# Kernel tuning notes

Measured on AMD Instinct MI355X. Metric: run time of the kernel, lower is better.

The kernel has to match this reference:

```python
import jax, jax.numpy as jnp
import numpy as np

ATT_UNITS = 64
DEC_DIM = 512
ENC_DIM = 512


def setup_inputs() -> dict:
    key = jax.random.key(0)
    k1, k2, k3, k4, k5 = jax.random.split(key, 5)
    B, S = 256, 512
    # glorot-uniform-ish init scales
    def glorot(k, shape):
        fan_in, fan_out = shape[0], shape[1]
        lim = np.sqrt(6.0 / (fan_in + fan_out))
        return jax.random.uniform(k, shape, jnp.float32, -lim, lim)
    return {
        "decoder_hidden_state": jax.random.normal(k1, (B, DEC_DIM), jnp.float32),
        "encoder_output": jax.random.normal(k2, (B, S, ENC_DIM), jnp.float32),
        "w1_kernel": glorot(k3, (DEC_DIM, ATT_UNITS)),
        "w1_bias": jnp.zeros((ATT_UNITS,), jnp.float32),
        "w2_kernel": glorot(k4, (ENC_DIM, ATT_UNITS)),
        "w2_bias": jnp.zeros((ATT_UNITS,), jnp.float32),
        "v_kernel": glorot(k5, (ATT_UNITS, 1)),
        "v_bias": jnp.zeros((1,), jnp.float32),
    }


def reference(decoder_hidden_state, encoder_output, w1_kernel, w1_bias,
              w2_kernel, w2_bias, v_kernel, v_bias):
    # dec proj: [B, 1, U]; enc proj: [B, S, U]
    dec = (decoder_hidden_state @ w1_kernel + w1_bias)[:, None, :]
    enc = jnp.einsum('bse,eu->bsu', encoder_output, w2_kernel) + w2_bias
    # score: [B, S, 1]
    score = jnp.tanh(dec + enc) @ v_kernel + v_bias
    att_weights = jax.nn.softmax(score, axis=1)  # softmax over sequence axis
    # weighted sum over S -> [B, E]
    context_vector = jnp.sum(att_weights * encoder_output, axis=1)
    return (context_vector, att_weights)
```

## Files before the change

kernel.cpp:

```cpp
#include <hip/hip_runtime.h>
#include <hip/hip_bf16.h>

constexpr int NB = 256;
constexpr int SQ = 512;
constexpr int ED = 512;
constexpr int DD = 512;
constexpr int UU = 64;
constexpr int NT = 32;

typedef __attribute__((ext_vector_type(8))) short bf16x8;
typedef __attribute__((ext_vector_type(4))) float f32x4;

__device__ __forceinline__ void stage16(const void* g, void* l) {
  __builtin_amdgcn_global_load_lds(
      (const __attribute__((address_space(1))) void*)g,
      (__attribute__((address_space(3))) void*)l, 16, 0, 0);
}

__device__ __forceinline__ unsigned short bf16_rne(float f) {
  unsigned int u = __float_as_uint(f);
  u += 0x7FFFu + ((u >> 16) & 1u);
  return (unsigned short)(u >> 16);
}

__device__ __forceinline__ unsigned int pack2(float lo, float hi) {
  __hip_bfloat162 h = __float22bfloat162_rn(make_float2(lo, hi));
  return *reinterpret_cast<unsigned int*>(&h);
}

constexpr size_t WS_DEC   = 131072;
constexpr size_t WS_LBUF  = 196608;
constexpr size_t WS_CTILE = 262144;

__global__ __launch_bounds__(256) void prep_all(
    const float* __restrict__ w2, unsigned short* __restrict__ wsb,
    const float* __restrict__ dh, const float* __restrict__ w1,
    const float* __restrict__ w1b, const float* __restrict__ w2b,
    float* __restrict__ dec_ws) {
  const int blk = blockIdx.x;
  __shared__ float red[256];
  if (blk < 128) {
    int tid = blk * 256 + threadIdx.x;
    int j    = tid & 7;
    int lane = (tid >> 3) & 63;
    int nt   = (tid >> 9) & 3;
    int ks   = tid >> 11;
    int e = ks * 32 + (lane >> 4) * 8 + j;
    int u = nt * 16 + (lane & 15);
    wsb[tid] = bf16_rne(w2[e * UU + u]);
  } else {
    const int b = blk - 128;
    const int t = threadIdx.x;
    const int wave = t >> 6;
    const float* dhb = dh + (size_t)b * DD;
    const int e0 = wave * 128;
    float s = 0.f;
    #pragma unroll 8
    for (int i = 0; i < 128; ++i) {
      int e = e0 + i;
      s = fmaf(dhb[e], w1[e * UU + (t & 63)], s);
    }
    red[t] = s;
    __syncthreads();
    if (t < 64) {
      float d = w1b[t] + w2b[t] + red[t] + red[64 + t] + red[128 + t] + red[192 + t];
      dec_ws[b * UU + t] = d;
    }
  }
}

__global__ __launch_bounds__(256, 4) void attn_tile(
    const float* __restrict__ x,
    const float* __restrict__ vk,
    const unsigned short* __restrict__ wsb,
    const float* __restrict__ dec_ws,
    float* __restrict__ lbuf,
    float* __restrict__ ctile,
    float* __restrict__ out)
{
  const int bid = blockIdx.x;
  const int b  = bid >> 5;
  const int tl = bid & 31;
  const int t = threadIdx.x;
  const int wave = t >> 6;
  const int lane = t & 63;
  const int ul = lane & 15;
  const int g  = lane >> 4;
  const int swz = (ul & 7) << 4;
  const int kw = wave >> 1;
  const int nw = wave & 1;

  __shared__ __align__(16) unsigned char slab[16][2048];
  __shared__ __align__(16) f32x4 red4[4][64];
  __shared__ float psum[2][16];

  const char* gsrc = (const char*)x + (size_t)(b * SQ + tl * 16) * 2048;

  #pragma unroll
  for (int r = 0; r < 4; ++r) {
    int row = wave * 4 + r;
    #pragma unroll
    for (int h = 0; h < 2; ++h) {
      int off = h * 1024 + lane * 16;
      stage16(gsrc + (size_t)row * 2048 + (size_t)(off ^ ((row & 7) << 4)),
              &slab[row][off]);
    }
  }

  const unsigned short* bp = wsb + lane * 8;
  bf16x8 bf[8][2];
  #pragma unroll
  for (int i = 0; i < 8; ++i) {
    #pragma unroll
    for (int j = 0; j < 2; ++j)
      bf[i][j] = *(const bf16x8*)(bp + (kw * 8 + i) * 2048 + (nw * 2 + j) * 512);
  }
  float dvs[2], vvs[2];
  #pragma unroll
  for (int j = 0; j < 2; ++j) {
    dvs[j] = dec_ws[b * UU + (nw * 2 + j) * 16 + ul];
    vvs[j] = vk[(nw * 2 + j) * 16 + ul];
  }
  float av = fabsf(vk[lane]);
  av += __shfl_xor(av, 1);
  av += __shfl_xor(av, 2);
  av += __shfl_xor(av, 4);
  av += __shfl_xor(av, 8);
  av += __shfl_xor(av, 16);
  av += __shfl_xor(av, 32);
  const float M = av;

  __syncthreads();

  const f32x4 zero4 = {0.f, 0.f, 0.f, 0.f};
  f32x4 acc[2];
  acc[0] = zero4;
  acc[1] = zero4;

  const unsigned char* Ab = &slab[ul][0];
  #pragma unroll
  for (int i = 0; i < 8; ++i) {
    const int k = kw * 8 + i;
    f32x4 a0 = *(const f32x4*)(Ab + ((g * 32 + k * 128) ^ swz));
    f32x4 a1 = *(const f32x4*)(Ab + ((g * 32 + k * 128 + 16) ^ swz));
    unsigned int w4[4];
    w4[0] = pack2(a0[0], a0[1]);
    w4[1] = pack2(a0[2], a0[3]);
    w4[2] = pack2(a1[0], a1[1]);
    w4[3] = pack2(a1[2], a1[3]);
    bf16x8 ahi;
    memcpy(&ahi, w4, 16);
    acc[0] = __builtin_amdgcn_mfma_f32_16x16x32_bf16(ahi, bf[i][0], acc[0], 0, 0, 0);
    acc[1] = __builtin_amdgcn_mfma_f32_16x16x32_bf16(ahi, bf[i][1], acc[1], 0, 0, 0);
  }

  if (kw == 0) {
    red4[nw * 2 + 0][lane] = acc[0];
    red4[nw * 2 + 1][lane] = acc[1];
  }
  __syncthreads();
  if (kw == 1) {
    #pragma unroll
    for (int j = 0; j < 2; ++j) {
      f32x4 o = red4[nw * 2 + j][lane];
      acc[j][0] += o[0];
      acc[j][1] += o[1];
      acc[j][2] += o[2];
      acc[j][3] += o[3];
    }
    #pragma unroll
    for (int r = 0; r < 4; ++r) {
      float s = 0.f;
      #pragma unroll
      for (int j = 0; j < 2; ++j) {
        float z = acc[j][r] + dvs[j];
        float ez = __expf(2.f * z);
        float th = 1.f - 2.f / (ez + 1.f);
        s = fmaf(th, vvs[j], s);
      }
      s += __shfl_xor(s, 1);
      s += __shfl_xor(s, 2);
      s += __shfl_xor(s, 4);
      s += __shfl_xor(s, 8);
      if (ul == 0) psum[nw][g * 4 + r] = s;
    }
  }
  __syncthreads();

  float p[4];
  float lsum = 0.f;
  #pragma unroll
  for (int r = 0; r < 4; ++r) {
    int row = g * 4 + r;
    float sc = psum[0][row] + psum[1][row];
    p[r] = __expf(sc - M);
    lsum += p[r];
  }
  lsum += __shfl_xor(lsum, 16);
  lsum += __shfl_xor(lsum, 32);
  lsum += __shfl_xor(lsum, 1);
  lsum += __shfl_xor(lsum, 2);
  lsum += __shfl_xor(lsum, 4);
  lsum += __shfl_xor(lsum, 8);
  lsum *= 0.0625f;

  if (wave == 0 && ul == 0) {
    float* att = out + (size_t)NB * ED + (size_t)b * SQ + tl * 16;
    #pragma unroll
    for (int r = 0; r < 4; ++r) att[g * 4 + r] = p[r];
  }
  if (t == 0) lbuf[b * NT + tl] = lsum;

  {
    const int cbase = wave * 512 + lane * 8;
    float cx = 0.f, cy = 0.f;
    #pragma unroll
    for (int rr = 0; rr < 16; ++rr) {
      const float2 v = *(const float2*)&slab[rr][cbase ^ ((rr & 7) << 4)];
      float pi = __shfl(p[rr & 3], (rr >> 2) << 4);
      cx = fmaf(pi, v.x, cx);
      cy = fmaf(pi, v.y, cy);
    }
    float* ct = ctile + ((size_t)b * NT + tl) * ED + wave * 128 + lane * 2;
    ct[0] = cx;
    ct[1] = cy;
  }
}

__global__ __launch_bounds__(256) void combine(
    const float* __restrict__ lbuf,
    const float* __restrict__ ctile, float* __restrict__ out) {
  const int b = blockIdx.x;
  const int t = threadIdx.x;

  float L = 0.f;
  #pragma unroll 8
  for (int j = 0; j < NT; ++j) L += lbuf[b * NT + j];
  const float inv = 1.f / L;

  float* att = out + (size_t)NB * ED + (size_t)b * SQ;
  #pragma unroll
  for (int s = t; s < SQ; s += 256) att[s] *= inv;

  const float* ct = ctile + (size_t)b * NT * ED;
  #pragma unroll
  for (int e = t; e < ED; e += 256) {
    float c = 0.f;
    #pragma unroll 8
    for (int j = 0; j < NT; ++j) c += ct[j * ED + e];
    out[(size_t)b * ED + e] = c * inv;
  }
}

extern "C" void kernel_launch(void* const* d_in, const int* in_sizes, int n_in,
                              void* d_out, int out_size, void* d_ws, size_t ws_size,
                              hipStream_t stream) {
  const float* dh  = (const float*)d_in[0];
  const float* x   = (const float*)d_in[1];
  const float* w1  = (const float*)d_in[2];
  const float* w1b = (const float*)d_in[3];
  const float* w2  = (const float*)d_in[4];
  const float* w2b = (const float*)d_in[5];
  const float* vk  = (const float*)d_in[6];
  unsigned short* wsb = (unsigned short*)d_ws;
  float* dec_ws = (float*)((char*)d_ws + WS_DEC);
  float* lbuf   = (float*)((char*)d_ws + WS_LBUF);
  float* ctile  = (float*)((char*)d_ws + WS_CTILE);
  float* out = (float*)d_out;

  prep_all<<<384, 256, 0, stream>>>(w2, wsb, dh, w1, w1b, w2b, dec_ws);
  attn_tile<<<NB * NT, 256, 0, stream>>>(x, vk, wsb, dec_ws, lbuf, ctile, out);
  combine<<<NB, 256, 0, stream>>>(lbuf, ctile, out);
}
```

Baseline: 79.31 us.

## Split MFMA work by N across waves instead of split-K with LDS reduction

```diff
diff --git a/kernel.cpp b/kernel.cpp
--- a/kernel.cpp
+++ b/kernel.cpp
@@ -87,12 +87,9 @@
   const int ul = lane & 15;
   const int g  = lane >> 4;
   const int swz = (ul & 7) << 4;
-  const int kw = wave >> 1;
-  const int nw = wave & 1;
 
   __shared__ __align__(16) unsigned char slab[16][2048];
-  __shared__ __align__(16) f32x4 red4[4][64];
-  __shared__ float psum[2][16];
+  __shared__ float psum[4][16];
 
   const char* gsrc = (const char*)x + (size_t)(b * SQ + tl * 16) * 2048;
 
@@ -107,20 +104,12 @@
     }
   }
 
-  const unsigned short* bp = wsb + lane * 8;
-  bf16x8 bf[8][2];
-  #pragma unroll
-  for (int i = 0; i < 8; ++i) {
-    #pragma unroll
-    for (int j = 0; j < 2; ++j)
-      bf[i][j] = *(const bf16x8*)(bp + (kw * 8 + i) * 2048 + (nw * 2 + j) * 512);
-  }
-  float dvs[2], vvs[2];
-  #pragma unroll
-  for (int j = 0; j < 2; ++j) {
-    dvs[j] = dec_ws[b * UU + (nw * 2 + j) * 16 + ul];
-    vvs[j] = vk[(nw * 2 + j) * 16 + ul];
-  }
+  const unsigned short* bp = wsb + wave * 512 + lane * 8;
+  bf16x8 bf[16];
+  #pragma unroll
+  for (int k = 0; k < 16; ++k) bf[k] = *(const bf16x8*)(bp + k * 2048);
+  const float dvs = dec_ws[b * UU + wave * 16 + ul];
+  const float vvs = vk[wave * 16 + ul];
   float av = fabsf(vk[lane]);
   av += __shfl_xor(av, 1);
   av += __shfl_xor(av, 2);
@@ -133,14 +122,11 @@
   __syncthreads();
 
   const f32x4 zero4 = {0.f, 0.f, 0.f, 0.f};
-  f32x4 acc[2];
-  acc[0] = zero4;
-  acc[1] = zero4;
+  f32x4 acc = zero4;
 
   const unsigned char* Ab = &slab[ul][0];
   #pragma unroll
-  for (int i = 0; i < 8; ++i) {
-    const int k = kw * 8 + i;
+  for (int k = 0; k < 16; ++k) {
     f32x4 a0 = *(const f32x4*)(Ab + ((g * 32 + k * 128) ^ swz));
     f32x4 a1 = *(const f32x4*)(Ab + ((g * 32 + k * 128 + 16) ^ swz));
     unsigned int w4[4];
@@ -150,40 +136,20 @@
     w4[3] = pack2(a1[2], a1[3]);
     bf16x8 ahi;
     memcpy(&ahi, w4, 16);
-    acc[0] = __builtin_amdgcn_mfma_f32_16x16x32_bf16(ahi, bf[i][0], acc[0], 0, 0, 0);
-    acc[1] = __builtin_amdgcn_mfma_f32_16x16x32_bf16(ahi, bf[i][1], acc[1], 0, 0, 0);
-  }
-
-  if (kw == 0) {
-    red4[nw * 2 + 0][lane] = acc[0];
-    red4[nw * 2 + 1][lane] = acc[1];
-  }
-  __syncthreads();
-  if (kw == 1) {
-    #pragma unroll
-    for (int j = 0; j < 2; ++j) {
-      f32x4 o = red4[nw * 2 + j][lane];
-      acc[j][0] += o[0];
-      acc[j][1] += o[1];
-      acc[j][2] += o[2];
-      acc[j][3] += o[3];
-    }
-    #pragma unroll
-    for (int r = 0; r < 4; ++r) {
-      float s = 0.f;
-      #pragma unroll
-      for (int j = 0; j < 2; ++j) {
-        float z = acc[j][r] + dvs[j];
-        float ez = __expf(2.f * z);
-        float th = 1.f - 2.f / (ez + 1.f);
-        s = fmaf(th, vvs[j], s);
-      }
-      s += __shfl_xor(s, 1);
-      s += __shfl_xor(s, 2);
-      s += __shfl_xor(s, 4);
-      s += __shfl_xor(s, 8);
-      if (ul == 0) psum[nw][g * 4 + r] = s;
-    }
+    acc = __builtin_amdgcn_mfma_f32_16x16x32_bf16(ahi, bf[k], acc, 0, 0, 0);
+  }
+
+  #pragma unroll
+  for (int r = 0; r < 4; ++r) {
+    float z = acc[r] + dvs;
+    float ez = __expf(2.f * z);
+    float th = 1.f - 2.f / (ez + 1.f);
+    float s = th * vvs;
+    s += __shfl_xor(s, 1);
+    s += __shfl_xor(s, 2);
+    s += __shfl_xor(s, 4);
+    s += __shfl_xor(s, 8);
+    if (ul == 0) psum[wave][g * 4 + r] = s;
   }
   __syncthreads();
 
@@ -192,7 +158,7 @@
   #pragma unroll
   for (int r = 0; r < 4; ++r) {
     int row = g * 4 + r;
-    float sc = psum[0][row] + psum[1][row];
+    float sc = psum[0][row] + psum[1][row] + psum[2][row] + psum[3][row];
     p[r] = __expf(sc - M);
     lsum += p[r];
   }
```

Result: slower. 83.87 us (+5.8%).

## Make attention blocks persistent over four tiles with double-buffered LDS staging

Applied to the files above, without the earlier changes.

```diff
diff --git a/kernel.cpp b/kernel.cpp
--- a/kernel.cpp
+++ b/kernel.cpp
@@ -10,6 +10,12 @@
 
 typedef __attribute__((ext_vector_type(8))) short bf16x8;
 typedef __attribute__((ext_vector_type(4))) float f32x4;
+
+#define MEMFENCE asm volatile("" ::: "memory")
+#define SBAR do { MEMFENCE; __builtin_amdgcn_s_barrier(); MEMFENCE; } while (0)
+#define WAITVM(n) asm volatile("s_waitcnt vmcnt(" #n ")" ::: "memory")
+#define WAITLGKM do { asm volatile("s_waitcnt lgkmcnt(0)" ::: "memory"); \
+                      __builtin_amdgcn_sched_barrier(0); } while (0)
 
 __device__ __forceinline__ void stage16(const void* g, void* l) {
   __builtin_amdgcn_global_load_lds(
@@ -69,7 +75,7 @@
   }
 }
 
-__global__ __launch_bounds__(256, 4) void attn_tile(
+__global__ __launch_bounds__(256, 2) void attn_tile(
     const float* __restrict__ x,
     const float* __restrict__ vk,
     const unsigned short* __restrict__ wsb,
@@ -78,9 +84,8 @@
     float* __restrict__ ctile,
     float* __restrict__ out)
 {
-  const int bid = blockIdx.x;
-  const int b  = bid >> 5;
-  const int tl = bid & 31;
+  const int b  = blockIdx.x >> 3;
+  const int q8 = blockIdx.x & 7;
   const int t = threadIdx.x;
   const int wave = t >> 6;
   const int lane = t & 63;
@@ -90,22 +95,11 @@
   const int kw = wave >> 1;
   const int nw = wave & 1;
 
-  __shared__ __align__(16) unsigned char slab[16][2048];
+  __shared__ __align__(16) unsigned char slab[2][16][2048];
   __shared__ __align__(16) f32x4 red4[4][64];
   __shared__ float psum[2][16];
 
-  const char* gsrc = (const char*)x + (size_t)(b * SQ + tl * 16) * 2048;
-
-  #pragma unroll
-  for (int r = 0; r < 4; ++r) {
-    int row = wave * 4 + r;
-    #pragma unroll
-    for (int h = 0; h < 2; ++h) {
-      int off = h * 1024 + lane * 16;
-      stage16(gsrc + (size_t)row * 2048 + (size_t)(off ^ ((row & 7) << 4)),
-              &slab[row][off]);
-    }
-  }
+  const char* gbase = (const char*)x + (size_t)(b * SQ + q8 * 64) * 2048;
 
   const unsigned short* bp = wsb + lane * 8;
   bf16x8 bf[8][2];
@@ -130,100 +124,126 @@
   av += __shfl_xor(av, 32);
   const float M = av;
 
-  __syncthreads();
+  auto stageT = [&](int i, int buf) {
+    #pragma unroll
+    for (int r = 0; r < 4; ++r) {
+      int row = wave * 4 + r;
+      #pragma unroll
+      for (int h = 0; h < 2; ++h) {
+        int off = h * 1024 + lane * 16;
+        stage16(gbase + (size_t)(i * 16 + row) * 2048 + (size_t)(off ^ ((row & 7) << 4)),
+                &slab[buf][row][off]);
+      }
+    }
+  };
+
+  stageT(0, 0);
+  stageT(1, 1);
 
   const f32x4 zero4 = {0.f, 0.f, 0.f, 0.f};
-  f32x4 acc[2];
-  acc[0] = zero4;
-  acc[1] = zero4;
-
-  const unsigned char* Ab = &slab[ul][0];
-  #pragma unroll
-  for (int i = 0; i < 8; ++i) {
-    const int k = kw * 8 + i;
-    f32x4 a0 = *(const f32x4*)(Ab + ((g * 32 + k * 128) ^ swz));
-    f32x4 a1 = *(const f32x4*)(Ab + ((g * 32 + k * 128 + 16) ^ swz));
-    unsigned int w4[4];
-    w4[0] = pack2(a0[0], a0[1]);
-    w4[1] = pack2(a0[2], a0[3]);
-    w4[2] = pack2(a1[0], a1[1]);
-    w4[3] = pack2(a1[2], a1[3]);
-    bf16x8 ahi;
-    memcpy(&ahi, w4, 16);
-    acc[0] = __builtin_amdgcn_mfma_f32_16x16x32_bf16(ahi, bf[i][0], acc[0], 0, 0, 0);
-    acc[1] = __builtin_amdgcn_mfma_f32_16x16x32_bf16(ahi, bf[i][1], acc[1], 0, 0, 0);
-  }
-
-  if (kw == 0) {
-    red4[nw * 2 + 0][lane] = acc[0];
-    red4[nw * 2 + 1][lane] = acc[1];
-  }
-  __syncthreads();
-  if (kw == 1) {
-    #pragma unroll
-    for (int j = 0; j < 2; ++j) {
-      f32x4 o = red4[nw * 2 + j][lane];
-      acc[j][0] += o[0];
-      acc[j][1] += o[1];
-      acc[j][2] += o[2];
-      acc[j][3] += o[3];
-    }
+
+  #pragma unroll
+  for (int i = 0; i < 4; ++i) {
+    if (i < 3) { WAITVM(8); } else { WAITVM(0); }
+    SBAR;
+    const int buf = i & 1;
+    const int tl = q8 * 4 + i;
+
+    f32x4 acc[2];
+    acc[0] = zero4;
+    acc[1] = zero4;
+    const unsigned char* Ab = &slab[buf][ul][0];
+    #pragma unroll
+    for (int i2 = 0; i2 < 8; ++i2) {
+      const int k = kw * 8 + i2;
+      f32x4 a0 = *(const f32x4*)(Ab + ((g * 32 + k * 128) ^ swz));
+      f32x4 a1 = *(const f32x4*)(Ab + ((g * 32 + k * 128 + 16) ^ swz));
+      unsigned int w4[4];
+      w4[0] = pack2(a0[0], a0[1]);
+      w4[1] = pack2(a0[2], a0[3]);
+      w4[2] = pack2(a1[0], a1[1]);
+      w4[3] = pack2(a1[2], a1[3]);
+      bf16x8 ahi;
+      memcpy(&ahi, w4, 16);
+      acc[0] = __builtin_amdgcn_mfma_f32_16x16x32_bf16(ahi, bf[i2][0], acc[0], 0, 0, 0);
+      acc[1] = __builtin_amdgcn_mfma_f32_16x16x32_bf16(ahi, bf[i2][1], acc[1], 0, 0, 0);
+    }
+
+    if (kw == 0) {
+      red4[nw * 2 + 0][lane] = acc[0];
+      red4[nw * 2 + 1][lane] = acc[1];
+    }
+    WAITLGKM;
+    SBAR;
+    if (kw == 1) {
+      #pragma unroll
+      for (int j = 0; j < 2; ++j) {
+        f32x4 o = red4[nw * 2 + j][lane];
+        acc[j][0] += o[0];
+        acc[j][1] += o[1];
+        acc[j][2] += o[2];
+        acc[j][3] += o[3];
+      }
+      #pragma unroll
+      for (int r = 0; r < 4; ++r) {
+        float s = 0.f;
+        #pragma unroll
+        for (int j = 0; j < 2; ++j) {
+          float z = acc[j][r] + dvs[j];
+          float ez = __expf(2.f * z);
+          float th = 1.f - 2.f / (ez + 1.f);
+          s = fmaf(th, vvs[j], s);
+        }
+        s += __shfl_xor(s, 1);
+        s += __shfl_xor(s, 2);
+        s += __shfl_xor(s, 4);
+        s += __shfl_xor(s, 8);
+        if (ul == 0) psum[nw][g * 4 + r] = s;
+      }
+    }
+    WAITLGKM;
+    SBAR;
+
+    float p[4];
+    float lsum = 0.f;
     #pragma unroll
     for (int r = 0; r < 4; ++r) {
-      float s = 0.f;
-      #pragma unroll
-      for (int j = 0; j < 2; ++j) {
-        float z = acc[j][r] + dvs[j];
-        float ez = __expf(2.f * z);
-        float th = 1.f - 2.f / (ez + 1.f);
-        s = fmaf(th, vvs[j], s);
-      }
-      s += __shfl_xor(s, 1);
-      s += __shfl_xor(s, 2);
-      s += __shfl_xor(s, 4);
-      s += __shfl_xor(s, 8);
-      if (ul == 0) psum[nw][g * 4 + r] = s;
-    }
-  }
-  __syncthreads();
-
-  float p[4];
-  float lsum = 0.f;
-  #pragma unroll
-  for (int r = 0; r < 4; ++r) {
-    int row = g * 4 + r;
-    float sc = psum[0][row] + psum[1][row];
-    p[r] = __expf(sc - M);
-    lsum += p[r];
-  }
-  lsum += __shfl_xor(lsum, 16);
-  lsum += __shfl_xor(lsum, 32);
-  lsum += __shfl_xor(lsum, 1);
-  lsum += __shfl_xor(lsum, 2);
-  lsum += __shfl_xor(lsum, 4);
-  lsum += __shfl_xor(lsum, 8);
-  lsum *= 0.0625f;
-
-  if (wave == 0 && ul == 0) {
-    float* att = out + (size_t)NB * ED + (size_t)b * SQ + tl * 16;
-    #pragma unroll
-    for (int r = 0; r < 4; ++r) att[g * 4 + r] = p[r];
-  }
-  if (t == 0) lbuf[b * NT + tl] = lsum;
-
-  {
-    const int cbase = wave * 512 + lane * 8;
-    float cx = 0.f, cy = 0.f;
-    #pragma unroll
-    for (int rr = 0; rr < 16; ++rr) {
-      const float2 v = *(const float2*)&slab[rr][cbase ^ ((rr & 7) << 4)];
-      float pi = __shfl(p[rr & 3], (rr >> 2) << 4);
-      cx = fmaf(pi, v.x, cx);
-      cy = fmaf(pi, v.y, cy);
-    }
-    float* ct = ctile + ((size_t)b * NT + tl) * ED + wave * 128 + lane * 2;
-    ct[0] = cx;
-    ct[1] = cy;
+      int row = g * 4 + r;
+      float sc = psum[0][row] + psum[1][row];
+      p[r] = __expf(sc - M);
+      lsum += p[r];
+    }
+    lsum += __shfl_xor(lsum, 16);
+    lsum += __shfl_xor(lsum, 32);
+    lsum += __shfl_xor(lsum, 1);
+    lsum += __shfl_xor(lsum, 2);
+    lsum += __shfl_xor(lsum, 4);
+    lsum += __shfl_xor(lsum, 8);
+    lsum *= 0.0625f;
+
+    if (wave == 0 && ul == 0) {
+      float* att = out + (size_t)NB * ED + (size_t)b * SQ + tl * 16;
+      #pragma unroll
+      for (int r = 0; r < 4; ++r) att[g * 4 + r] = p[r];
+    }
+    if (t == 0) lbuf[b * NT + tl] = lsum;
+
+    {
+      const int cbase = wave * 512 + lane * 8;
+      float cx = 0.f, cy = 0.f;
+      #pragma unroll
+      for (int rr = 0; rr < 16; ++rr) {
+        const float2 v = *(const float2*)&slab[buf][rr][cbase ^ ((rr & 7) << 4)];
+        float pi = __shfl(p[rr & 3], (rr >> 2) << 4);
+        cx = fmaf(pi, v.x, cx);
+        cy = fmaf(pi, v.y, cy);
+      }
+      float* ct = ctile + ((size_t)b * NT + tl) * ED + wave * 128 + lane * 2;
+      *(float2*)ct = make_float2(cx, cy);
+    }
+
+    SBAR;
+    if (i < 2) stageT(i + 2, buf);
   }
 }
 
@@ -269,6 +289,6 @@
   float* out = (float*)d_out;
 
   prep_all<<<384, 256, 0, stream>>>(w2, wsb, dh, w1, w1b, w2b, dec_ws);
-  attn_tile<<<NB * NT, 256, 0, stream>>>(x, vk, wsb, dec_ws, lbuf, ctile, out);
+  attn_tile<<<NB * 8, 256, 0, stream>>>(x, vk, wsb, dec_ws, lbuf, ctile, out);
   combine<<<NB, 256, 0, stream>>>(lbuf, ctile, out);
 }
```

Measured after the change: 92.14 us. 16.2% more time.
